# Kernel tuning notes

Hardware: AMD Instinct MI355X
Metric: run time of the kernel (lower is better)

## Reference

```python
import jax, jax.numpy as jnp
import numpy as np

N_HEADS = 8
EMBED = 512
N_LAYERS = 3
FF = 2048
IN_DIM = 256
BATCH = 32
GRAPH = 512
HEAD_DIM = EMBED // N_HEADS  # key_dim == val_dim == 64
BN_EPS = 1e-5


def setup_inputs() -> dict:
    key = jax.random.key(0)
    ks = jax.random.split(key, 16)
    u = lambda k, shape, fan: jax.random.uniform(k, shape, jnp.float32, -1.0, 1.0) / np.sqrt(fan)
    inp = {
        "x": jax.random.normal(ks[0], (BATCH, GRAPH, IN_DIM), jnp.float32),
        # init_embed Linear(graphsage_output_dim -> embed_dim)
        "W_init": u(ks[1], (IN_DIM, EMBED), IN_DIM),
        "b_init": u(ks[2], (EMBED,), IN_DIM),
        "eot": jnp.zeros((1, 1, EMBED), jnp.float32),  # end_of_token parameter
        # stacked per-layer MHA params (uniform(-1/sqrt(last_dim), ...) as in init_parameters)
        "Wq": u(ks[3], (N_LAYERS, N_HEADS, EMBED, HEAD_DIM), HEAD_DIM),
        "Wk": u(ks[4], (N_LAYERS, N_HEADS, EMBED, HEAD_DIM), HEAD_DIM),
        "Wv": u(ks[5], (N_LAYERS, N_HEADS, EMBED, HEAD_DIM), HEAD_DIM),
        "Wo": u(ks[6], (N_LAYERS, N_HEADS, HEAD_DIM, EMBED), EMBED),
        # BatchNorm affine params (BN1 after attention skip, BN2 after FFN skip)
        "bn1_g": jnp.ones((N_LAYERS, EMBED), jnp.float32),
        "bn1_b": jnp.zeros((N_LAYERS, EMBED), jnp.float32),
        "W1": u(ks[7], (N_LAYERS, EMBED, FF), EMBED),
        "b1": u(ks[8], (N_LAYERS, FF), EMBED),
        "W2": u(ks[9], (N_LAYERS, FF, EMBED), FF),
        "b2": u(ks[10], (N_LAYERS, EMBED), FF),
        "bn2_g": jnp.ones((N_LAYERS, EMBED), jnp.float32),
        "bn2_b": jnp.zeros((N_LAYERS, EMBED), jnp.float32),
    }
    return inp


def _mha(h, Wq, Wk, Wv, Wo):
    # h: [b, n, d]; Wq/Wk/Wv: [H, d, k]; Wo: [H, k, d]
    scale = float(HEAD_DIM) ** -0.5
    Q = jnp.einsum("bnd,hdk->hbnk", h, Wq)
    K = jnp.einsum("bnd,hdk->hbnk", h, Wk)
    V = jnp.einsum("bnd,hdk->hbnk", h, Wv)
    attn = jax.nn.softmax(jnp.einsum("hbqk,hbnk->hbqn", Q, K) * scale, axis=-1)
    heads = jnp.einsum("hbqn,hbnk->hbqk", attn, V)
    return jnp.einsum("hbqk,hkd->bqd", heads, Wo)


def _batchnorm(h, gamma, beta):
    # BatchNorm1d in train mode over flattened (batch*seq, embed)
    hf = h.reshape(-1, h.shape[-1])
    m = hf.mean(axis=0)
    v = hf.var(axis=0)  # biased variance, as in torch BN normalization
    return ((hf - m) * jax.lax.rsqrt(v + BN_EPS) * gamma + beta).reshape(h.shape)


def reference(x, W_init, b_init, eot, Wq, Wk, Wv, Wo, bn1_g, bn1_b, W1, b1, W2, b2, bn2_g, bn2_b):
    h = x @ W_init + b_init                                   # [b, n, d]
    eot_b = jnp.broadcast_to(eot, (h.shape[0], 1, h.shape[-1]))
    h = jnp.concatenate([h, eot_b], axis=1)                   # [b, n+1, d]
    for i in range(N_LAYERS):
        h = _batchnorm(h + _mha(h, Wq[i], Wk[i], Wv[i], Wo[i]), bn1_g[i], bn1_b[i])
        ff = jax.nn.relu(h @ W1[i] + b1[i]) @ W2[i] + b2[i]
        h = _batchnorm(h + ff, bn2_g[i], bn2_b[i])
    return h
```

## Files before the change

### kernel.cpp

```cpp
#include <hip/hip_runtime.h>
#include <stdint.h>

typedef unsigned short u16;
typedef __attribute__((ext_vector_type(8))) short bfrag;
typedef __attribute__((ext_vector_type(4))) float f32x4;

#define MFMA16(a,b,c) __builtin_amdgcn_mfma_f32_16x16x32_bf16(a,b,c,0,0,0)

__device__ __forceinline__ u16 f2b(float f){
  union { float f; uint32_t u; } v; v.f = f;
  uint32_t r = v.u + 0x7FFFu + ((v.u >> 16) & 1u);
  return (u16)(r >> 16);
}

typedef const __attribute__((address_space(1))) unsigned int* gas_t;
typedef __attribute__((address_space(3))) unsigned int* las_t;
__device__ __forceinline__ void async16(const u16* g, u16* l){
  __builtin_amdgcn_global_load_lds((gas_t)g, (las_t)l, 16, 0, 0);
}

__global__ __launch_bounds__(256) void cvt_x_k(const float* __restrict__ x, u16* __restrict__ o, int n){
  int i = blockIdx.x*256 + threadIdx.x;
  if (i < n) o[i] = f2b(x[i]);
}
__global__ __launch_bounds__(256) void cvt_winit_k(const float* __restrict__ w, u16* __restrict__ o){
  int i = blockIdx.x*256 + threadIdx.x;
  int n = i >> 8, k = i & 255;
  o[i] = f2b(w[k*512 + n]);
}
__global__ __launch_bounds__(256) void cvt_qkv_k(const float* __restrict__ Wq, const float* __restrict__ Wk,
                                                 const float* __restrict__ Wv, u16* __restrict__ o){
  int i = blockIdx.x*256 + threadIdx.x;
  int d = i & 511;
  int j = (i >> 9) % 1536;
  int l = i / (1536*512);
  int which = j >> 9, hk = j & 511, h = hk >> 6, k = hk & 63;
  const float* W = which==0 ? Wq : (which==1 ? Wk : Wv);
  o[i] = f2b(W[(((size_t)l*8 + h)*512 + d)*64 + k]);
}
__global__ __launch_bounds__(256) void cvt_wo_k(const float* __restrict__ W, u16* __restrict__ o){
  int i = blockIdx.x*256 + threadIdx.x;
  int hk = i & 511;
  int dout = (i >> 9) & 511;
  int l = i >> 18;
  int h = hk >> 6, k = hk & 63;
  o[i] = f2b(W[(((size_t)l*8 + h)*64 + k)*512 + dout]);
}
__global__ __launch_bounds__(256) void cvt_w1_k(const float* __restrict__ W, u16* __restrict__ o){
  int i = blockIdx.x*256 + threadIdx.x;
  int d = i & 511;
  int f = (i >> 9) & 2047;
  int l = i >> 20;
  o[i] = f2b(W[((size_t)l*512 + d)*2048 + f]);
}
__global__ __launch_bounds__(256) void cvt_w2_k(const float* __restrict__ W, u16* __restrict__ o){
  int i = blockIdx.x*256 + threadIdx.x;
  int f = i & 2047;
  int d = (i >> 11) & 511;
  int l = i >> 20;
  o[i] = f2b(W[((size_t)l*2048 + f)*512 + d]);
}
__global__ __launch_bounds__(256) void eot_k(const float* __restrict__ eot, float* __restrict__ hF, u16* __restrict__ hbf){
  int i = blockIdx.x*256 + threadIdx.x;
  int b = i >> 9, d = i & 511;
  float v = eot[d];
  size_t idx = ((size_t)b*513 + 512)*512 + d;
  hF[idx] = v; hbf[idx] = f2b(v);
}

template<bool BIAS,bool RELU,bool SKIP,bool OUTF,bool OUTB,bool REMAP>
__global__ __launch_bounds__(256,2) void gemm_k(
    const u16* __restrict__ A, const u16* __restrict__ BT,
    const float* __restrict__ bias, const float* __restrict__ skip,
    float* __restrict__ outF, u16* __restrict__ outB,
    int M, int N, int K)
{
  __shared__ u16 Ash[128*32];
  __shared__ u16 Bsh[128*32];
  const int tid = threadIdx.x;
  const int lane = tid & 63, wv = tid >> 6;
  const int mt = blockIdx.x, nt = blockIdx.y;
  const int wrow = (wv >> 1) << 6, wcol = (wv & 1) << 6;
  const int g = lane >> 4, ci = lane & 15;

  f32x4 acc[4][4];
  #pragma unroll
  for (int i=0;i<4;i++)
    #pragma unroll
    for (int j=0;j<4;j++) acc[i][j] = (f32x4){0.f,0.f,0.f,0.f};

  int aoff[4], boff[4];
  #pragma unroll
  for (int mi=0;mi<4;mi++){
    int rr = wrow + mi*16 + ci;
    aoff[mi] = (rr*4 + (g ^ (rr&3) ^ ((rr>>2)&1)))*8;
    int cc = wcol + mi*16 + ci;
    boff[mi] = (cc*4 + (g ^ (cc&3) ^ ((cc>>2)&1)))*8;
  }
  const int o0 = tid, o1 = 256 + tid;
  const int ra0 = o0>>2, ca0 = o0&3, ra1 = o1>>2, ca1 = o1&3;
  const int sa0 = ca0 ^ (ra0&3) ^ ((ra0>>2)&1);
  const int sa1 = ca1 ^ (ra1&3) ^ ((ra1>>2)&1);
  int arow0 = mt*128 + ra0; if (arow0 >= M) arow0 = M-1;
  int arow1 = mt*128 + ra1; if (arow1 >= M) arow1 = M-1;
  const int brow0 = nt*128 + ra0, brow1 = nt*128 + ra1;
  const u16* ga0 = A + (size_t)arow0*K + sa0*8;
  const u16* ga1 = A + (size_t)arow1*K + sa1*8;
  const u16* gb0 = BT + (size_t)brow0*K + sa0*8;
  const u16* gb1 = BT + (size_t)brow1*K + sa1*8;
  u16* la0 = &Ash[(      wv*64)*8];
  u16* la1 = &Ash[(256 + wv*64)*8];
  u16* lb0 = &Bsh[(      wv*64)*8];
  u16* lb1 = &Bsh[(256 + wv*64)*8];

  for (int kt = 0; kt < K; kt += 32){
    async16(ga0 + kt, la0);
    async16(ga1 + kt, la1);
    async16(gb0 + kt, lb0);
    async16(gb1 + kt, lb1);
    __syncthreads();
    bfrag a[4], b[4];
    #pragma unroll
    for (int mi=0;mi<4;mi++) a[mi] = *(const bfrag*)&Ash[aoff[mi]];
    #pragma unroll
    for (int ni=0;ni<4;ni++) b[ni] = *(const bfrag*)&Bsh[boff[ni]];
    #pragma unroll
    for (int mi=0;mi<4;mi++)
      #pragma unroll
      for (int ni=0;ni<4;ni++)
        acc[mi][ni] = MFMA16(a[mi], b[ni], acc[mi][ni]);
    __syncthreads();
  }

  #pragma unroll
  for (int mi=0;mi<4;mi++){
    #pragma unroll
    for (int r=0;r<4;r++){
      int gm = mt*128 + wrow + mi*16 + g*4 + r;
      if (gm >= M) continue;
      size_t orow = REMAP ? (size_t)(gm + (gm >> 9)) : (size_t)gm;
      #pragma unroll
      for (int ni=0;ni<4;ni++){
        int gn = nt*128 + wcol + ni*16 + ci;
        float v = acc[mi][ni][r];
        if (BIAS) v += bias[gn];
        if (SKIP) v += skip[(size_t)gm*N + gn];
        if (RELU) v = fmaxf(v, 0.f);
        if (OUTF) outF[orow*N + gn] = v;
        if (OUTB) outB[orow*N + gn] = f2b(v);
      }
    }
  }
}

__global__ __launch_bounds__(64) void attn_k(const u16* __restrict__ qkv, u16* __restrict__ heads)
{
  const int qt = blockIdx.x, b = blockIdx.y, hh = blockIdx.z;
  const int lane = threadIdx.x;
  const int g = lane >> 4, ci = lane & 15;
  __shared__ u16 P_lds[16*40];
  __shared__ u16 V_lds[32*64];

  const size_t rowb = (size_t)b * 513;
  int q = qt*16 + ci; int qr = q < 513 ? q : 512;
  const u16* qp = qkv + (rowb + qr)*1536 + hh*64 + g*8;
  bfrag aq0 = *(const bfrag*)qp;
  bfrag aq1 = *(const bfrag*)(qp + 32);

  f32x4 hacc[4];
  #pragma unroll
  for (int dt=0;dt<4;dt++) hacc[dt] = (f32x4){0.f,0.f,0.f,0.f};
  float mrun[4] = {-1e30f,-1e30f,-1e30f,-1e30f};
  float srun[4] = {0.f,0.f,0.f,0.f};

  for (int np = 0; np < 17; ++np){
    int n0 = np*32;
    #pragma unroll
    for (int i=0;i<4;i++){
      int o = i*64 + lane;
      int r = o >> 3, c = o & 7;
      int n = n0 + r; int nr = n < 513 ? n : 512;
      async16(qkv + (rowb + nr)*1536 + 1024 + hh*64 + c*8, &V_lds[i*64*8]);
    }
    int n_a = n0 + ci, n_b = n0 + 16 + ci;
    int nra = n_a < 513 ? n_a : 512, nrb = n_b < 513 ? n_b : 512;
    const u16* kpa = qkv + (rowb + nra)*1536 + 512 + hh*64 + g*8;
    const u16* kpb = qkv + (rowb + nrb)*1536 + 512 + hh*64 + g*8;
    bfrag k0a = *(const bfrag*)kpa, k1a = *(const bfrag*)(kpa+32);
    bfrag k0b = *(const bfrag*)kpb, k1b = *(const bfrag*)(kpb+32);
    f32x4 s0 = (f32x4){0.f,0.f,0.f,0.f}, s1 = (f32x4){0.f,0.f,0.f,0.f};
    s0 = MFMA16(aq0, k0a, s0); s0 = MFMA16(aq1, k1a, s0);
    s1 = MFMA16(aq0, k0b, s1); s1 = MFMA16(aq1, k1b, s1);
    const bool va = n_a < 513, vb = n_b < 513;
    float pm[4];
    #pragma unroll
    for (int r=0;r<4;r++){
      s0[r] = va ? s0[r]*0.125f : -1e30f;
      s1[r] = vb ? s1[r]*0.125f : -1e30f;
      pm[r] = fmaxf(s0[r], s1[r]);
    }
    #pragma unroll
    for (int m=1;m<16;m<<=1){
      #pragma unroll
      for (int r=0;r<4;r++) pm[r] = fmaxf(pm[r], __shfl_xor(pm[r], m));
    }
    float f[4], psum[4];
    f32x4 p0, p1;
    #pragma unroll
    for (int r=0;r<4;r++){
      float mn = fmaxf(mrun[r], pm[r]);
      f[r] = __expf(mrun[r] - mn);
      mrun[r] = mn;
      p0[r] = __expf(s0[r] - mn);
      p1[r] = __expf(s1[r] - mn);
      psum[r] = p0[r] + p1[r];
    }
    #pragma unroll
    for (int m=1;m<16;m<<=1){
      #pragma unroll
      for (int r=0;r<4;r++) psum[r] += __shfl_xor(psum[r], m);
    }
    #pragma unroll
    for (int r=0;r<4;r++){
      srun[r] = srun[r]*f[r] + psum[r];
      P_lds[(g*4+r)*40 + ci]      = f2b(p0[r]);
      P_lds[(g*4+r)*40 + 16 + ci] = f2b(p1[r]);
    }
    #pragma unroll
    for (int dt=0;dt<4;dt++){
      hacc[dt][0]*=f[0]; hacc[dt][1]*=f[1]; hacc[dt][2]*=f[2]; hacc[dt][3]*=f[3];
    }
    __syncthreads();
    bfrag pa = *(const bfrag*)&P_lds[ci*40 + g*8];
    #pragma unroll
    for (int dt=0;dt<4;dt++){
      bfrag bv;
      #pragma unroll
      for (int j=0;j<8;j++) bv[j] = (short)V_lds[(g*8+j)*64 + dt*16 + ci];
      hacc[dt] = MFMA16(pa, bv, hacc[dt]);
    }
    __syncthreads();
  }
  #pragma unroll
  for (int dt=0;dt<4;dt++){
    #pragma unroll
    for (int r=0;r<4;r++){
      int qg = qt*16 + g*4 + r;
      if (qg < 513)
        heads[(rowb + qg)*512 + hh*64 + dt*16 + ci] = f2b(hacc[dt][r] / srun[r]);
    }
  }
}

#define NBSTAT 258
__global__ __launch_bounds__(256) void bn_stats_k(const float* __restrict__ in, float* __restrict__ p1, float* __restrict__ p2){
  int blk = blockIdx.x, t = threadIdx.x;
  int r0 = blk*64, r1 = r0+64 < 16416 ? r0+64 : 16416;
  float s0=0.f,q0=0.f,s1=0.f,q1=0.f;
  for (int r=r0;r<r1;r++){
    float a = in[(size_t)r*512 + t];       s0+=a; q0+=a*a;
    float b = in[(size_t)r*512 + 256 + t]; s1+=b; q1+=b*b;
  }
  p1[(size_t)t*NBSTAT + blk] = s0; p1[(size_t)(t+256)*NBSTAT + blk] = s1;
  p2[(size_t)t*NBSTAT + blk] = q0; p2[(size_t)(t+256)*NBSTAT + blk] = q1;
}
__global__ __launch_bounds__(256) void bn_fin_k(const float* __restrict__ p1, const float* __restrict__ p2,
                                               const float* __restrict__ gamma, const float* __restrict__ beta,
                                               float2* __restrict__ sc){
  int c = blockIdx.x*256 + threadIdx.x;
  float S=0.f,Q=0.f;
  for (int i=0;i<NBSTAT;i++){ S += p1[(size_t)c*NBSTAT+i]; Q += p2[(size_t)c*NBSTAT+i]; }
  const float invM = 1.0f/16416.0f;
  float mean = S*invM;
  float var  = Q*invM - mean*mean;
  float scl  = gamma[c] * rsqrtf(var + 1e-5f);
  sc[c] = make_float2(scl, beta[c] - mean*scl);
}
__global__ __launch_bounds__(256) void bn_apply_k(const float* __restrict__ in, const float2* __restrict__ sc,
                                                  float* __restrict__ outF, u16* __restrict__ outB){
  const int n4 = 16416*512/4;
  for (int i = blockIdx.x*256 + threadIdx.x; i < n4; i += gridDim.x*256){
    float4 v = ((const float4*)in)[i];
    int c0 = (i << 2) & 511;
    float2 a = sc[c0], b = sc[c0+1], c = sc[c0+2], d = sc[c0+3];
    v.x = v.x*a.x + a.y; v.y = v.y*b.x + b.y; v.z = v.z*c.x + c.y; v.w = v.w*d.x + d.y;
    ((float4*)outF)[i] = v;
    ushort4 u; u.x=f2b(v.x); u.y=f2b(v.y); u.z=f2b(v.z); u.w=f2b(v.w);
    ((ushort4*)outB)[i] = u;
  }
}

static inline size_t alignup(size_t x){ return (x + 255) & ~(size_t)255; }

extern "C" void kernel_launch(void* const* d_in, const int* in_sizes, int n_in,
                              void* d_out, int out_size, void* d_ws, size_t ws_size,
                              hipStream_t stream)
{
  (void)in_sizes; (void)n_in; (void)out_size; (void)ws_size;
  const float* x      = (const float*)d_in[0];
  const float* W_init = (const float*)d_in[1];
  const float* b_init = (const float*)d_in[2];
  const float* eot    = (const float*)d_in[3];
  const float* Wq     = (const float*)d_in[4];
  const float* Wk     = (const float*)d_in[5];
  const float* Wv     = (const float*)d_in[6];
  const float* Wo     = (const float*)d_in[7];
  const float* bn1g   = (const float*)d_in[8];
  const float* bn1b   = (const float*)d_in[9];
  const float* W1     = (const float*)d_in[10];
  const float* b1     = (const float*)d_in[11];
  const float* W2     = (const float*)d_in[12];
  const float* b2     = (const float*)d_in[13];
  const float* bn2g   = (const float*)d_in[14];
  const float* bn2b   = (const float*)d_in[15];

  char* ws = (char*)d_ws;
  size_t o = 0;
  u16*    hbf    = (u16*)  (ws + o); o += alignup(16416ull*512*2);
  float*  hF     = (float*)(ws + o); o += alignup(16416ull*512*4);
  float*  bufB   = (float*)(ws + o); o += alignup(16416ull*512*4);
  u16*    heads  = (u16*)  (ws + o); o += alignup(16416ull*512*2);
  u16*    big    = (u16*)  (ws + o); o += alignup(16416ull*2048*2);
  u16*    winitT = (u16*)  (ws + o); o += alignup(512ull*256*2);
  u16*    wqkvT  = (u16*)  (ws + o); o += alignup(3ull*1536*512*2);
  u16*    woT    = (u16*)  (ws + o); o += alignup(3ull*512*512*2);
  u16*    w1T    = (u16*)  (ws + o); o += alignup(3ull*2048*512*2);
  u16*    w2T    = (u16*)  (ws + o); o += alignup(3ull*512*2048*2);
  float*  p1     = (float*)(ws + o); o += alignup(512ull*NBSTAT*4);
  float*  p2     = (float*)(ws + o); o += alignup(512ull*NBSTAT*4);
  float2* scv    = (float2*)(ws + o); o += alignup(512*8);
  u16* xbf = big; u16* qkv = big; u16* ffb = big;

  cvt_x_k    <<<16384,256,0,stream>>>(x, xbf, 16384*256);
  cvt_winit_k<<<  512,256,0,stream>>>(W_init, winitT);
  cvt_qkv_k  <<< 9216,256,0,stream>>>(Wq, Wk, Wv, wqkvT);
  cvt_wo_k   <<< 3072,256,0,stream>>>(Wo, woT);
  cvt_w1_k   <<<12288,256,0,stream>>>(W1, w1T);
  cvt_w2_k   <<<12288,256,0,stream>>>(W2, w2T);

  gemm_k<true,false,false,true,true,true><<<dim3(128,4),256,0,stream>>>(
      xbf, winitT, b_init, nullptr, hF, hbf, 16384, 512, 256);
  eot_k<<<64,256,0,stream>>>(eot, hF, hbf);

  for (int l = 0; l < 3; ++l){
    gemm_k<false,false,false,false,true,false><<<dim3(129,12),256,0,stream>>>(
        hbf, wqkvT + (size_t)l*1536*512, nullptr, nullptr, nullptr, qkv, 16416, 1536, 512);
    attn_k<<<dim3(33,32,8),64,0,stream>>>(qkv, heads);
    gemm_k<false,false,true,true,false,false><<<dim3(129,4),256,0,stream>>>(
        heads, woT + (size_t)l*512*512, nullptr, hF, bufB, nullptr, 16416, 512, 512);
    bn_stats_k<<<NBSTAT,256,0,stream>>>(bufB, p1, p2);
    bn_fin_k  <<<2,256,0,stream>>>(p1, p2, bn1g + l*512, bn1b + l*512, scv);
    bn_apply_k<<<2048,256,0,stream>>>(bufB, scv, hF, hbf);
    gemm_k<true,true,false,false,true,false><<<dim3(129,16),256,0,stream>>>(
        hbf, w1T + (size_t)l*2048*512, b1 + l*2048, nullptr, nullptr, ffb, 16416, 2048, 512);
    gemm_k<true,false,true,true,false,false><<<dim3(129,4),256,0,stream>>>(
        ffb, w2T + (size_t)l*512*2048, b2 + l*512, hF, bufB, nullptr, 16416, 512, 2048);
    bn_stats_k<<<NBSTAT,256,0,stream>>>(bufB, p1, p2);
    bn_fin_k  <<<2,256,0,stream>>>(p1, p2, bn2g + l*512, bn2b + l*512, scv);
    bn_apply_k<<<2048,256,0,stream>>>(bufB, scv, (l==2) ? (float*)d_out : hF, hbf);
  }
}
```

Measured before the change: 1.582 ms.

## Widen GEMM K-tile, restructure attention with pre-transposed V, vectorize BN stats

The GEMM now stages a 64-wide K tile per iteration with an 8-way XOR swizzle, which halves the number of barrier-separated iterations. Attention runs four waves per block, processes 64 keys per step with exp2 and a folded scale, and reads V from a transposed copy made by a new tiled transpose kernel. That copy replaces the per-element strided LDS gathers and the block barriers. Weight conversion kernels are replaced by a shared-memory tiled transpose with coalesced accesses, and BN stats use float4 loads with more partial blocks. The trade-offs are an extra V transpose pass per layer, double the LDS use in the GEMM, and a cheaper rounding mode for the P values.

```diff
diff --git a/kernel.cpp b/kernel.cpp
--- a/kernel.cpp
+++ b/kernel.cpp
@@ -12,6 +12,13 @@
   uint32_t r = v.u + 0x7FFFu + ((v.u >> 16) & 1u);
   return (u16)(r >> 16);
 }
+__device__ __forceinline__ u16 f2b_fast(float f){
+  union { float f; uint32_t u; } v; v.f = f;
+  return (u16)((v.u + 0x8000u) >> 16);
+}
+__device__ __forceinline__ float b2f(u16 b){
+  union { uint32_t u; float f; } v; v.u = ((uint32_t)b) << 16; return v.f;
+}
 
 typedef const __attribute__((address_space(1))) unsigned int* gas_t;
 typedef __attribute__((address_space(3))) unsigned int* las_t;
@@ -22,43 +29,6 @@
 __global__ __launch_bounds__(256) void cvt_x_k(const float* __restrict__ x, u16* __restrict__ o, int n){
   int i = blockIdx.x*256 + threadIdx.x;
   if (i < n) o[i] = f2b(x[i]);
-}
-__global__ __launch_bounds__(256) void cvt_winit_k(const float* __restrict__ w, u16* __restrict__ o){
-  int i = blockIdx.x*256 + threadIdx.x;
-  int n = i >> 8, k = i & 255;
-  o[i] = f2b(w[k*512 + n]);
-}
-__global__ __launch_bounds__(256) void cvt_qkv_k(const float* __restrict__ Wq, const float* __restrict__ Wk,
-                                                 const float* __restrict__ Wv, u16* __restrict__ o){
-  int i = blockIdx.x*256 + threadIdx.x;
-  int d = i & 511;
-  int j = (i >> 9) % 1536;
-  int l = i / (1536*512);
-  int which = j >> 9, hk = j & 511, h = hk >> 6, k = hk & 63;
-  const float* W = which==0 ? Wq : (which==1 ? Wk : Wv);
-  o[i] = f2b(W[(((size_t)l*8 + h)*512 + d)*64 + k]);
-}
-__global__ __launch_bounds__(256) void cvt_wo_k(const float* __restrict__ W, u16* __restrict__ o){
-  int i = blockIdx.x*256 + threadIdx.x;
-  int hk = i & 511;
-  int dout = (i >> 9) & 511;
-  int l = i >> 18;
-  int h = hk >> 6, k = hk & 63;
-  o[i] = f2b(W[(((size_t)l*8 + h)*64 + k)*512 + dout]);
-}
-__global__ __launch_bounds__(256) void cvt_w1_k(const float* __restrict__ W, u16* __restrict__ o){
-  int i = blockIdx.x*256 + threadIdx.x;
-  int d = i & 511;
-  int f = (i >> 9) & 2047;
-  int l = i >> 20;
-  o[i] = f2b(W[((size_t)l*512 + d)*2048 + f]);
-}
-__global__ __launch_bounds__(256) void cvt_w2_k(const float* __restrict__ W, u16* __restrict__ o){
-  int i = blockIdx.x*256 + threadIdx.x;
-  int f = i & 2047;
-  int d = (i >> 11) & 511;
-  int l = i >> 20;
-  o[i] = f2b(W[((size_t)l*2048 + f)*512 + d]);
 }
 __global__ __launch_bounds__(256) void eot_k(const float* __restrict__ eot, float* __restrict__ hF, u16* __restrict__ hbf){
   int i = blockIdx.x*256 + threadIdx.x;
@@ -66,6 +36,50 @@
   float v = eot[d];
   size_t idx = ((size_t)b*513 + 512)*512 + d;
   hF[idx] = v; hbf[idx] = f2b(v);
+}
+
+template<typename T>
+__global__ __launch_bounds__(256) void trans_k(const T* __restrict__ src, u16* __restrict__ dst,
+    int R, int C, int SS, int DS, int div, size_t srcA, size_t srcB, size_t dstA, size_t dstB)
+{
+  __shared__ u16 tile[64][72];
+  int s = blockIdx.z;
+  const T* sp = src + (size_t)(s/div)*srcA + (size_t)(s%div)*srcB;
+  u16* dp = dst + (size_t)(s/div)*dstA + (size_t)(s%div)*dstB;
+  int r0 = blockIdx.x*64, c0 = blockIdx.y*64;
+  int t = threadIdx.x;
+  int tr = t>>2, tc = (t&3)*16;
+  int rr = r0+tr; if (rr >= R) rr = R-1;
+  const T* p = sp + (size_t)rr*SS + c0 + tc;
+  u16 bv[16];
+  if constexpr (sizeof(T)==4) {
+    float4 a = *(const float4*)p, b = *(const float4*)(p+4),
+           c = *(const float4*)(p+8), d = *(const float4*)(p+12);
+    float f[16] = {a.x,a.y,a.z,a.w,b.x,b.y,b.z,b.w,c.x,c.y,c.z,c.w,d.x,d.y,d.z,d.w};
+    #pragma unroll
+    for (int i=0;i<16;i++) bv[i] = f2b(f[i]);
+  } else {
+    *(uint4*)&bv[0] = ((const uint4*)p)[0];
+    *(uint4*)&bv[8] = ((const uint4*)p)[1];
+  }
+  *(uint4*)&tile[tr][tc]   = *(uint4*)&bv[0];
+  *(uint4*)&tile[tr][tc+8] = *(uint4*)&bv[8];
+  __syncthreads();
+  int oc = t>>2, orr = (t&3)*16;
+  u16 ov[16];
+  #pragma unroll
+  for (int i=0;i<16;i++) ov[i] = tile[orr+i][oc];
+  u16* q = dp + (size_t)(c0+oc)*DS + r0 + orr;
+  if (r0 + 64 <= R) {
+    *(uint4*)q     = *(uint4*)&ov[0];
+    *(uint4*)(q+8) = *(uint4*)&ov[8];
+  } else {
+    #pragma unroll
+    for (int i=0;i<16;i++){
+      int rg = r0 + orr + i;
+      if (rg < DS) q[i] = (rg < R) ? ov[i] : (u16)0;
+    }
+  }
 }
 
 template<bool BIAS,bool RELU,bool SKIP,bool OUTF,bool OUTB,bool REMAP>
@@ -75,8 +89,8 @@
     float* __restrict__ outF, u16* __restrict__ outB,
     int M, int N, int K)
 {
-  __shared__ u16 Ash[128*32];
-  __shared__ u16 Bsh[128*32];
+  __shared__ u16 Ash[128*64];
+  __shared__ u16 Bsh[128*64];
   const int tid = threadIdx.x;
   const int lane = tid & 63, wv = tid >> 6;
   const int mt = blockIdx.x, nt = blockIdx.y;
@@ -89,46 +103,49 @@
     #pragma unroll
     for (int j=0;j<4;j++) acc[i][j] = (f32x4){0.f,0.f,0.f,0.f};
 
-  int aoff[4], boff[4];
+  int aofs[4][2], bofs[4][2];
   #pragma unroll
   for (int mi=0;mi<4;mi++){
     int rr = wrow + mi*16 + ci;
-    aoff[mi] = (rr*4 + (g ^ (rr&3) ^ ((rr>>2)&1)))*8;
     int cc = wcol + mi*16 + ci;
-    boff[mi] = (cc*4 + (g ^ (cc&3) ^ ((cc>>2)&1)))*8;
-  }
-  const int o0 = tid, o1 = 256 + tid;
-  const int ra0 = o0>>2, ca0 = o0&3, ra1 = o1>>2, ca1 = o1&3;
-  const int sa0 = ca0 ^ (ra0&3) ^ ((ra0>>2)&1);
-  const int sa1 = ca1 ^ (ra1&3) ^ ((ra1>>2)&1);
-  int arow0 = mt*128 + ra0; if (arow0 >= M) arow0 = M-1;
-  int arow1 = mt*128 + ra1; if (arow1 >= M) arow1 = M-1;
-  const int brow0 = nt*128 + ra0, brow1 = nt*128 + ra1;
-  const u16* ga0 = A + (size_t)arow0*K + sa0*8;
-  const u16* ga1 = A + (size_t)arow1*K + sa1*8;
-  const u16* gb0 = BT + (size_t)brow0*K + sa0*8;
-  const u16* gb1 = BT + (size_t)brow1*K + sa1*8;
-  u16* la0 = &Ash[(      wv*64)*8];
-  u16* la1 = &Ash[(256 + wv*64)*8];
-  u16* lb0 = &Bsh[(      wv*64)*8];
-  u16* lb1 = &Bsh[(256 + wv*64)*8];
-
-  for (int kt = 0; kt < K; kt += 32){
-    async16(ga0 + kt, la0);
-    async16(ga1 + kt, la1);
-    async16(gb0 + kt, lb0);
-    async16(gb1 + kt, lb1);
+    #pragma unroll
+    for (int kh=0;kh<2;kh++){
+      aofs[mi][kh] = rr*64 + ((((kh<<2)|g) ^ (rr&7))<<3);
+      bofs[mi][kh] = cc*64 + ((((kh<<2)|g) ^ (cc&7))<<3);
+    }
+  }
+  const u16* ga[4]; const u16* gb[4];
+  #pragma unroll
+  for (int q=0;q<4;q++){
+    int row = q*32 + (tid>>3);
+    int sc  = (tid&7) ^ (row&7);
+    int arow = mt*128 + row; if (arow >= M) arow = M-1;
+    int brow = nt*128 + row;
+    ga[q] = A  + (size_t)arow*K + sc*8;
+    gb[q] = BT + (size_t)brow*K + sc*8;
+  }
+  u16* la = Ash + tid*8;
+  u16* lb = Bsh + tid*8;
+
+  for (int kt = 0; kt < K; kt += 64){
+    #pragma unroll
+    for (int q=0;q<4;q++) async16(ga[q] + kt, la + q*2048);
+    #pragma unroll
+    for (int q=0;q<4;q++) async16(gb[q] + kt, lb + q*2048);
     __syncthreads();
-    bfrag a[4], b[4];
-    #pragma unroll
-    for (int mi=0;mi<4;mi++) a[mi] = *(const bfrag*)&Ash[aoff[mi]];
-    #pragma unroll
-    for (int ni=0;ni<4;ni++) b[ni] = *(const bfrag*)&Bsh[boff[ni]];
-    #pragma unroll
-    for (int mi=0;mi<4;mi++)
-      #pragma unroll
-      for (int ni=0;ni<4;ni++)
-        acc[mi][ni] = MFMA16(a[mi], b[ni], acc[mi][ni]);
+    #pragma unroll
+    for (int kh=0;kh<2;kh++){
+      bfrag a[4], b[4];
+      #pragma unroll
+      for (int mi=0;mi<4;mi++) a[mi] = *(const bfrag*)&Ash[aofs[mi][kh]];
+      #pragma unroll
+      for (int ni=0;ni<4;ni++) b[ni] = *(const bfrag*)&Bsh[bofs[ni][kh]];
+      #pragma unroll
+      for (int mi=0;mi<4;mi++)
+        #pragma unroll
+        for (int ni=0;ni<4;ni++)
+          acc[mi][ni] = MFMA16(a[mi], b[ni], acc[mi][ni]);
+    }
     __syncthreads();
   }
 
@@ -153,13 +170,18 @@
   }
 }
 
-__global__ __launch_bounds__(64) void attn_k(const u16* __restrict__ qkv, u16* __restrict__ heads)
+#define LOG2E_SC 0.1803368801f
+__global__ __launch_bounds__(256) void attn_k(const u16* __restrict__ qkv, const u16* __restrict__ Vt,
+                                              u16* __restrict__ heads)
 {
-  const int qt = blockIdx.x, b = blockIdx.y, hh = blockIdx.z;
-  const int lane = threadIdx.x;
+  __shared__ u16 P_lds[4][16*72];
+  const int wv = threadIdx.x >> 6;
+  const int qt = blockIdx.x*4 + wv;
+  if (qt > 32) return;
+  const int b = blockIdx.y, hh = blockIdx.z;
+  const int lane = threadIdx.x & 63;
   const int g = lane >> 4, ci = lane & 15;
-  __shared__ u16 P_lds[16*40];
-  __shared__ u16 V_lds[32*64];
+  u16* P_l = P_lds[wv];
 
   const size_t rowb = (size_t)b * 513;
   int q = qt*16 + ci; int qr = q < 513 ? q : 512;
@@ -167,109 +189,129 @@
   bfrag aq0 = *(const bfrag*)qp;
   bfrag aq1 = *(const bfrag*)(qp + 32);
 
+  const u16* kbase = qkv + rowb*1536 + 512 + hh*64;
+  const u16* vbase = Vt + (size_t)(b*8 + hh)*33280;
+
   f32x4 hacc[4];
   #pragma unroll
   for (int dt=0;dt<4;dt++) hacc[dt] = (f32x4){0.f,0.f,0.f,0.f};
   float mrun[4] = {-1e30f,-1e30f,-1e30f,-1e30f};
   float srun[4] = {0.f,0.f,0.f,0.f};
 
-  for (int np = 0; np < 17; ++np){
-    int n0 = np*32;
-    #pragma unroll
-    for (int i=0;i<4;i++){
-      int o = i*64 + lane;
-      int r = o >> 3, c = o & 7;
-      int n = n0 + r; int nr = n < 513 ? n : 512;
-      async16(qkv + (rowb + nr)*1536 + 1024 + hh*64 + c*8, &V_lds[i*64*8]);
-    }
-    int n_a = n0 + ci, n_b = n0 + 16 + ci;
-    int nra = n_a < 513 ? n_a : 512, nrb = n_b < 513 ? n_b : 512;
-    const u16* kpa = qkv + (rowb + nra)*1536 + 512 + hh*64 + g*8;
-    const u16* kpb = qkv + (rowb + nrb)*1536 + 512 + hh*64 + g*8;
-    bfrag k0a = *(const bfrag*)kpa, k1a = *(const bfrag*)(kpa+32);
-    bfrag k0b = *(const bfrag*)kpb, k1b = *(const bfrag*)(kpb+32);
-    f32x4 s0 = (f32x4){0.f,0.f,0.f,0.f}, s1 = (f32x4){0.f,0.f,0.f,0.f};
-    s0 = MFMA16(aq0, k0a, s0); s0 = MFMA16(aq1, k1a, s0);
-    s1 = MFMA16(aq0, k0b, s1); s1 = MFMA16(aq1, k1b, s1);
-    const bool va = n_a < 513, vb = n_b < 513;
+  for (int np = 0; np < 9; ++np){
+    const int n0 = np*64;
+    const bool tail = (np == 8);
+    bfrag kf[4][2];
+    #pragma unroll
+    for (int t=0;t<4;t++){
+      int n = n0 + t*16 + ci; if (n > 512) n = 512;
+      const u16* kp = kbase + (size_t)n*1536;
+      kf[t][0] = *(const bfrag*)(kp + g*8);
+      kf[t][1] = *(const bfrag*)(kp + 32 + g*8);
+    }
+    bfrag vf[4][2];
+    #pragma unroll
+    for (int dt=0;dt<4;dt++){
+      const u16* vr = vbase + (size_t)(dt*16 + ci)*520;
+      #pragma unroll
+      for (int kh=0;kh<2;kh++){
+        int nv = tail ? 512 : (n0 + kh*32 + g*8);
+        vf[dt][kh] = *(const bfrag*)(vr + nv);
+      }
+    }
+    f32x4 s[4];
+    #pragma unroll
+    for (int t=0;t<4;t++){
+      f32x4 z = (f32x4){0.f,0.f,0.f,0.f};
+      z = MFMA16(aq0, kf[t][0], z);
+      z = MFMA16(aq1, kf[t][1], z);
+      #pragma unroll
+      for (int r=0;r<4;r++) s[t][r] = z[r]*LOG2E_SC;
+    }
+    if (tail){
+      #pragma unroll
+      for (int t=0;t<4;t++){
+        bool v = (n0 + t*16 + ci) < 513;
+        #pragma unroll
+        for (int r=0;r<4;r++) s[t][r] = v ? s[t][r] : -1e30f;
+      }
+    }
     float pm[4];
     #pragma unroll
-    for (int r=0;r<4;r++){
-      s0[r] = va ? s0[r]*0.125f : -1e30f;
-      s1[r] = vb ? s1[r]*0.125f : -1e30f;
-      pm[r] = fmaxf(s0[r], s1[r]);
-    }
-    #pragma unroll
-    for (int m=1;m<16;m<<=1){
+    for (int r=0;r<4;r++)
+      pm[r] = fmaxf(fmaxf(s[0][r],s[1][r]), fmaxf(s[2][r],s[3][r]));
+    #pragma unroll
+    for (int m=1;m<16;m<<=1)
       #pragma unroll
       for (int r=0;r<4;r++) pm[r] = fmaxf(pm[r], __shfl_xor(pm[r], m));
-    }
-    float f[4], psum[4];
-    f32x4 p0, p1;
+    float f[4];
     #pragma unroll
     for (int r=0;r<4;r++){
       float mn = fmaxf(mrun[r], pm[r]);
-      f[r] = __expf(mrun[r] - mn);
+      f[r] = __builtin_exp2f(mrun[r] - mn);
       mrun[r] = mn;
-      p0[r] = __expf(s0[r] - mn);
-      p1[r] = __expf(s1[r] - mn);
-      psum[r] = p0[r] + p1[r];
-    }
-    #pragma unroll
-    for (int m=1;m<16;m<<=1){
+      #pragma unroll
+      for (int t=0;t<4;t++) s[t][r] = __builtin_exp2f(s[t][r] - mn);
+    }
+    float psum[4];
+    #pragma unroll
+    for (int r=0;r<4;r++) psum[r] = (s[0][r]+s[1][r]) + (s[2][r]+s[3][r]);
+    #pragma unroll
+    for (int m=1;m<16;m<<=1)
       #pragma unroll
       for (int r=0;r<4;r++) psum[r] += __shfl_xor(psum[r], m);
-    }
-    #pragma unroll
-    for (int r=0;r<4;r++){
-      srun[r] = srun[r]*f[r] + psum[r];
-      P_lds[(g*4+r)*40 + ci]      = f2b(p0[r]);
-      P_lds[(g*4+r)*40 + 16 + ci] = f2b(p1[r]);
-    }
+    #pragma unroll
+    for (int r=0;r<4;r++) srun[r] = srun[r]*f[r] + psum[r];
     #pragma unroll
     for (int dt=0;dt<4;dt++){
       hacc[dt][0]*=f[0]; hacc[dt][1]*=f[1]; hacc[dt][2]*=f[2]; hacc[dt][3]*=f[3];
     }
-    __syncthreads();
-    bfrag pa = *(const bfrag*)&P_lds[ci*40 + g*8];
+    #pragma unroll
+    for (int r=0;r<4;r++)
+      #pragma unroll
+      for (int t=0;t<4;t++)
+        P_l[(g*4+r)*72 + t*16 + ci] = f2b_fast(s[t][r]);
+    bfrag pa0 = *(const bfrag*)&P_l[ci*72 + g*8];
+    bfrag pa1 = *(const bfrag*)&P_l[ci*72 + 32 + g*8];
     #pragma unroll
     for (int dt=0;dt<4;dt++){
-      bfrag bv;
-      #pragma unroll
-      for (int j=0;j<8;j++) bv[j] = (short)V_lds[(g*8+j)*64 + dt*16 + ci];
-      hacc[dt] = MFMA16(pa, bv, hacc[dt]);
-    }
-    __syncthreads();
-  }
-  #pragma unroll
-  for (int dt=0;dt<4;dt++){
+      hacc[dt] = MFMA16(pa0, vf[dt][0], hacc[dt]);
+      hacc[dt] = MFMA16(pa1, vf[dt][1], hacc[dt]);
+    }
+  }
+  float rs[4];
+  #pragma unroll
+  for (int r=0;r<4;r++) rs[r] = 1.0f / srun[r];
+  #pragma unroll
+  for (int dt=0;dt<4;dt++)
     #pragma unroll
     for (int r=0;r<4;r++){
       int qg = qt*16 + g*4 + r;
       if (qg < 513)
-        heads[(rowb + qg)*512 + hh*64 + dt*16 + ci] = f2b(hacc[dt][r] / srun[r]);
-    }
-  }
-}
-
-#define NBSTAT 258
+        heads[(rowb + qg)*512 + hh*64 + dt*16 + ci] = f2b(hacc[dt][r]*rs[r]);
+    }
+}
+
+#define NB 1026
 __global__ __launch_bounds__(256) void bn_stats_k(const float* __restrict__ in, float* __restrict__ p1, float* __restrict__ p2){
   int blk = blockIdx.x, t = threadIdx.x;
-  int r0 = blk*64, r1 = r0+64 < 16416 ? r0+64 : 16416;
-  float s0=0.f,q0=0.f,s1=0.f,q1=0.f;
-  for (int r=r0;r<r1;r++){
-    float a = in[(size_t)r*512 + t];       s0+=a; q0+=a*a;
-    float b = in[(size_t)r*512 + 256 + t]; s1+=b; q1+=b*b;
-  }
-  p1[(size_t)t*NBSTAT + blk] = s0; p1[(size_t)(t+256)*NBSTAT + blk] = s1;
-  p2[(size_t)t*NBSTAT + blk] = q0; p2[(size_t)(t+256)*NBSTAT + blk] = q1;
+  int c4 = t & 127, rh = t >> 7;
+  float4 s = {0,0,0,0}, qq = {0,0,0,0};
+  for (int i = rh; i < 32; i += 2){
+    float4 v = ((const float4*)in)[(size_t)(blk*32 + i)*128 + c4];
+    s.x += v.x; s.y += v.y; s.z += v.z; s.w += v.w;
+    qq.x += v.x*v.x; qq.y += v.y*v.y; qq.z += v.z*v.z; qq.w += v.w*v.w;
+  }
+  size_t base = (size_t)(c4*4)*NB + blk*2 + rh;
+  p1[base] = s.x; p1[base+NB] = s.y; p1[base+2*NB] = s.z; p1[base+3*NB] = s.w;
+  p2[base] = qq.x; p2[base+NB] = qq.y; p2[base+2*NB] = qq.z; p2[base+3*NB] = qq.w;
 }
 __global__ __launch_bounds__(256) void bn_fin_k(const float* __restrict__ p1, const float* __restrict__ p2,
                                                const float* __restrict__ gamma, const float* __restrict__ beta,
                                                float2* __restrict__ sc){
   int c = blockIdx.x*256 + threadIdx.x;
   float S=0.f,Q=0.f;
-  for (int i=0;i<NBSTAT;i++){ S += p1[(size_t)c*NBSTAT+i]; Q += p2[(size_t)c*NBSTAT+i]; }
+  for (int i=0;i<NB;i++){ S += p1[(size_t)c*NB+i]; Q += p2[(size_t)c*NB+i]; }
   const float invM = 1.0f/16416.0f;
   float mean = S*invM;
   float var  = Q*invM - mean*mean;
@@ -326,17 +368,20 @@
   u16*    woT    = (u16*)  (ws + o); o += alignup(3ull*512*512*2);
   u16*    w1T    = (u16*)  (ws + o); o += alignup(3ull*2048*512*2);
   u16*    w2T    = (u16*)  (ws + o); o += alignup(3ull*512*2048*2);
-  float*  p1     = (float*)(ws + o); o += alignup(512ull*NBSTAT*4);
-  float*  p2     = (float*)(ws + o); o += alignup(512ull*NBSTAT*4);
+  float*  p1     = (float*)(ws + o); o += alignup(512ull*NB*4);
+  float*  p2     = (float*)(ws + o); o += alignup(512ull*NB*4);
   float2* scv    = (float2*)(ws + o); o += alignup(512*8);
   u16* xbf = big; u16* qkv = big; u16* ffb = big;
-
-  cvt_x_k    <<<16384,256,0,stream>>>(x, xbf, 16384*256);
-  cvt_winit_k<<<  512,256,0,stream>>>(W_init, winitT);
-  cvt_qkv_k  <<< 9216,256,0,stream>>>(Wq, Wk, Wv, wqkvT);
-  cvt_wo_k   <<< 3072,256,0,stream>>>(Wo, woT);
-  cvt_w1_k   <<<12288,256,0,stream>>>(W1, w1T);
-  cvt_w2_k   <<<12288,256,0,stream>>>(W2, w2T);
+  u16* VtB = (u16*)bufB;
+
+  cvt_x_k<<<16384,256,0,stream>>>(x, xbf, 16384*256);
+  trans_k<float><<<dim3(4,8,1),   256,0,stream>>>(W_init, winitT, 256, 512, 512, 256, 1, 131072, 0, 0, 0);
+  trans_k<float><<<dim3(8,1,24),  256,0,stream>>>(Wq, wqkvT,            512, 64, 64, 512, 8, 262144, 32768, 786432, 32768);
+  trans_k<float><<<dim3(8,1,24),  256,0,stream>>>(Wk, wqkvT + 262144,   512, 64, 64, 512, 8, 262144, 32768, 786432, 32768);
+  trans_k<float><<<dim3(8,1,24),  256,0,stream>>>(Wv, wqkvT + 524288,   512, 64, 64, 512, 8, 262144, 32768, 786432, 32768);
+  trans_k<float><<<dim3(1,8,24),  256,0,stream>>>(Wo, woT,  64, 512, 512, 512, 8, 262144, 32768, 262144, 64);
+  trans_k<float><<<dim3(8,32,3),  256,0,stream>>>(W1, w1T,  512, 2048, 2048, 512, 1, 1048576, 0, 1048576, 0);
+  trans_k<float><<<dim3(32,8,3),  256,0,stream>>>(W2, w2T,  2048, 512, 512, 2048, 1, 1048576, 0, 1048576, 0);
 
   gemm_k<true,false,false,true,true,true><<<dim3(128,4),256,0,stream>>>(
       xbf, winitT, b_init, nullptr, hF, hbf, 16384, 512, 256);
@@ -345,17 +390,18 @@
   for (int l = 0; l < 3; ++l){
     gemm_k<false,false,false,false,true,false><<<dim3(129,12),256,0,stream>>>(
         hbf, wqkvT + (size_t)l*1536*512, nullptr, nullptr, nullptr, qkv, 16416, 1536, 512);
-    attn_k<<<dim3(33,32,8),64,0,stream>>>(qkv, heads);
+    trans_k<u16><<<dim3(9,1,256),256,0,stream>>>(qkv + 1024, VtB, 513, 64, 1536, 520, 8, 787968, 64, 266240, 33280);
+    attn_k<<<dim3(9,32,8),256,0,stream>>>(qkv, VtB, heads);
     gemm_k<false,false,true,true,false,false><<<dim3(129,4),256,0,stream>>>(
         heads, woT + (size_t)l*512*512, nullptr, hF, bufB, nullptr, 16416, 512, 512);
-    bn_stats_k<<<NBSTAT,256,0,stream>>>(bufB, p1, p2);
+    bn_stats_k<<<513,256,0,stream>>>(bufB, p1, p2);
     bn_fin_k  <<<2,256,0,stream>>>(p1, p2, bn1g + l*512, bn1b + l*512, scv);
     bn_apply_k<<<2048,256,0,stream>>>(bufB, scv, hF, hbf);
     gemm_k<true,true,false,false,true,false><<<dim3(129,16),256,0,stream>>>(
         hbf, w1T + (size_t)l*2048*512, b1 + l*2048, nullptr, nullptr, ffb, 16416, 2048, 512);
     gemm_k<true,false,true,true,false,false><<<dim3(129,4),256,0,stream>>>(
         ffb, w2T + (size_t)l*512*2048, b2 + l*512, hF, bufB, nullptr, 16416, 512, 2048);
-    bn_stats_k<<<NBSTAT,256,0,stream>>>(bufB, p1, p2);
+    bn_stats_k<<<513,256,0,stream>>>(bufB, p1, p2);
     bn_fin_k  <<<2,256,0,stream>>>(p1, p2, bn2g + l*512, bn2b + l*512, scv);
     bn_apply_k<<<2048,256,0,stream>>>(bufB, scv, (l==2) ? (float*)d_out : hF, hbf);
   }
```

New measurement: 2.046 ms. 1.29x slower.
